# Kernel optimization log

Hardware: AMD Instinct MI355X
Metric: run time of the kernel (lower is better)

## Reference

```python
import jax, jax.numpy as jnp
import numpy as np

# Dims: L layers, batch B, seq S, model dim D, heads H, ffn FF
L, B, S, D, H = 8, 2, 1024, 1024, 16
FF = 4 * D
HD = D // H
EPS = 1e-5  # torch LayerNorm default


def setup_inputs() -> dict:
    key = jax.random.key(0)
    ks = jax.random.split(key, 6)
    g = lambda k, shape, s: jax.random.normal(k, shape, jnp.float32) * s
    return {
        "x": g(ks[0], (B, S, D), 1.0),
        # True = masked out (code passes ~attn_mask to F.sdpa): causal mask
        "attn_mask": jnp.triu(jnp.ones((S, S), bool), 1),
        "qkv_w": g(ks[1], (L, 3 * D, D), 0.02),
        "qkv_b": jnp.zeros((L, 3 * D), jnp.float32),
        "out_w": g(ks[2], (L, D, D), 0.02),
        "out_b": jnp.zeros((L, D), jnp.float32),
        "w1": g(ks[3], (L, FF, D), 0.02),
        "b1": jnp.zeros((L, FF), jnp.float32),
        "w2": g(ks[4], (L, D, FF), 0.02),
        "b2": jnp.zeros((L, D), jnp.float32),
        "ln1_w": jnp.ones((L, D), jnp.float32),
        "ln1_b": jnp.zeros((L, D), jnp.float32),
        "ln2_w": jnp.ones((L, D), jnp.float32),
        "ln2_b": jnp.zeros((L, D), jnp.float32),
    }


def _layer_norm(x, w, b):
    m = jnp.mean(x, axis=-1, keepdims=True)
    v = jnp.var(x, axis=-1, keepdims=True)
    return (x - m) * jax.lax.rsqrt(v + EPS) * w + b


def _block(x, mask, qw, qb, ow, ob, w1, b1, w2, b2, l1w, l1b, l2w, l2b):
    # fused QKV projection: [B,S,3D]
    qkv = jnp.einsum("bsd,ed->bse", x, qw) + qb
    q, k, v = jnp.split(qkv, 3, axis=-1)
    k_cache, v_cache = k, v  # caches are stored pre-head-split [B,S,D]
    to_heads = lambda t: t.reshape(B, S, H, HD).transpose(0, 2, 1, 3)
    qh, kh, vh = to_heads(q), to_heads(k), to_heads(v)
    scores = jnp.einsum("bhqd,bhkd->bhqk", qh, kh) / jnp.sqrt(jnp.float32(HD))
    scores = jnp.where(mask, -jnp.inf, scores)  # mask True = disallowed
    attn = jnp.einsum("bhqk,bhkd->bhqd", jax.nn.softmax(scores, axis=-1), vh)
    attn = attn.transpose(0, 2, 1, 3).reshape(B, S, D)
    attn = jnp.einsum("bsd,ed->bse", attn, ow) + ob
    # post-LN residual + ReLU MLP + post-LN (padding_mask=None branch)
    x = _layer_norm(x + attn, l1w, l1b)
    h = jnp.einsum("bsf,df->bsd", jax.nn.relu(jnp.einsum("bsd,fd->bsf", x, w1) + b1), w2) + b2
    x = _layer_norm(x + h, l2w, l2b)
    return x, k_cache, v_cache


def reference(x, attn_mask, qkv_w, qkv_b, out_w, out_b, w1, b1, w2, b2,
              ln1_w, ln1_b, ln2_w, ln2_b):
    def step(carry, p):
        xc = carry
        xo, kc, vc = _block(xc, attn_mask, *p)
        return xo, (kc, vc)

    params = (qkv_w, qkv_b, out_w, out_b, w1, b1, w2, b2,
              ln1_w, ln1_b, ln2_w, ln2_b)
    x_out, (k_cache, v_cache) = jax.lax.scan(step, x, params)
    return x_out, k_cache, v_cache
```

## Files before the change

kernel.cpp:

```cpp
#include <hip/hip_runtime.h>
#include <cstdint>
#include <cstddef>
#include <math.h>

#define LL  8
#define BB  2
#define SS  1024
#define DD  1024
#define HH  16
#define HD  64
#define FFD 4096
#define BSD (BB*SS*DD)

typedef __attribute__((ext_vector_type(4))) float f32x4;
typedef __attribute__((ext_vector_type(8))) short bf16x8;
typedef __attribute__((ext_vector_type(4))) short bf16x4;

__device__ __forceinline__ unsigned short f2bf(float f) {
    unsigned u = __float_as_uint(f);
    unsigned r = (u + 0x7fffu + ((u >> 16) & 1u)) >> 16;
    return (unsigned short)r;
}
__device__ __forceinline__ float bf2f(unsigned short u) {
    return __uint_as_float((unsigned)u << 16);
}

#define GLD16(gsrc, ldst) \
    __builtin_amdgcn_global_load_lds((const __attribute__((address_space(1))) void*)(gsrc), \
                                     (__attribute__((address_space(3))) void*)(ldst), 16, 0, 0)

__global__ __launch_bounds__(256)
void cvt_bf16(const float* __restrict__ in, unsigned short* __restrict__ out)
{
    size_t i = (size_t)blockIdx.x * 256 + threadIdx.x;
    float4 v = *(const float4*)(in + i * 4);
    ushort4 o;
    o.x = f2bf(v.x); o.y = f2bf(v.y); o.z = f2bf(v.z); o.w = f2bf(v.w);
    *(ushort4*)(out + i * 4) = o;
}

__global__ __launch_bounds__(256)
void cvt_x(const float* __restrict__ in, float* __restrict__ outf,
           unsigned short* __restrict__ outb)
{
    size_t i = (size_t)blockIdx.x * 256 + threadIdx.x;
    float4 v = *(const float4*)(in + i * 4);
    *(float4*)(outf + i * 4) = v;
    ushort4 o;
    o.x = f2bf(v.x); o.y = f2bf(v.y); o.z = f2bf(v.z); o.w = f2bf(v.w);
    *(ushort4*)(outb + i * 4) = o;
}

__global__ __launch_bounds__(512)
void gemm_bf16(const unsigned short* __restrict__ A, const unsigned short* __restrict__ W,
               const float* __restrict__ bias,
               float* __restrict__ C, unsigned short* __restrict__ Cb,
               float* __restrict__ Ck, float* __restrict__ Cv,
               unsigned short* __restrict__ Kb16, unsigned short* __restrict__ Vb16,
               int M, int N, int klen, int mode)
{
    __shared__ unsigned short lds[2][2 * 128 * 64];

    const int tid  = threadIdx.x;
    const int m0   = blockIdx.y * 128;
    const int n0   = blockIdx.x * 128;
    const int kbase= blockIdx.z * klen;
    const int lane = tid & 63;
    const int w    = tid >> 6;
    const int wr   = w >> 2;
    const int wc   = w & 3;
    const int lr   = lane & 15;
    const int kq   = lane >> 4;

    const int K = (mode == 3) ? (klen * gridDim.z) : klen;
    const int T = klen >> 6;

    const int srow0 = tid >> 3;
    const int spc0  = tid & 7;
    const int slc0  = spc0 ^ (srow0 & 7);
    const int srow1 = (tid + 512) >> 3;
    const int spc1  = (tid + 512) & 7;
    const int slc1  = spc1 ^ (srow1 & 7);

    #define STAGE_TILE(ti, dst)                                                   \
        do {                                                                      \
            const int kc = kbase + (ti) * 64;                                     \
            GLD16(A + (size_t)(m0 + srow0) * K + kc + slc0 * 8, (dst) + tid * 8); \
            GLD16(A + (size_t)(m0 + srow1) * K + kc + slc1 * 8, (dst) + 4096 + tid * 8); \
            GLD16(W + (size_t)(n0 + srow0) * K + kc + slc0 * 8, (dst) + 8192 + tid * 8); \
            GLD16(W + (size_t)(n0 + srow1) * K + kc + slc1 * 8, (dst) + 12288 + tid * 8); \
        } while (0)

    f32x4 acc[4][2];
    #pragma unroll
    for (int i = 0; i < 4; ++i)
        #pragma unroll
        for (int j = 0; j < 2; ++j) {
            f32x4 z = {0.f, 0.f, 0.f, 0.f};
            acc[i][j] = z;
        }

    STAGE_TILE(0, lds[0]);
    STAGE_TILE(1, lds[1]);

    for (int t = 0; t < T; ++t) {
        unsigned short* cb = lds[t & 1];

        if (t == T - 1) {
            asm volatile("s_waitcnt vmcnt(0)\n\ts_barrier" ::: "memory");
        } else {
            asm volatile("s_waitcnt vmcnt(4)\n\ts_barrier" ::: "memory");
        }

        bf16x8 a[4], b[2];
        #pragma unroll
        for (int mf = 0; mf < 4; ++mf) {
            const int r = wr * 64 + mf * 16 + lr;
            const int pc = kq ^ (r & 7);
            a[mf] = *(const bf16x8*)(cb + r * 64 + pc * 8);
        }
        #pragma unroll
        for (int nf = 0; nf < 2; ++nf) {
            const int r = wc * 32 + nf * 16 + lr;
            const int pc = kq ^ (r & 7);
            b[nf] = *(const bf16x8*)(cb + 8192 + r * 64 + pc * 8);
        }
        bf16x8 a2[4], b2[2];
        #pragma unroll
        for (int mf = 0; mf < 4; ++mf) {
            const int r = wr * 64 + mf * 16 + lr;
            const int pc = (4 + kq) ^ (r & 7);
            a2[mf] = *(const bf16x8*)(cb + r * 64 + pc * 8);
        }
        #pragma unroll
        for (int nf = 0; nf < 2; ++nf) {
            const int r = wc * 32 + nf * 16 + lr;
            const int pc = (4 + kq) ^ (r & 7);
            b2[nf] = *(const bf16x8*)(cb + 8192 + r * 64 + pc * 8);
        }

        asm volatile("s_waitcnt lgkmcnt(0)\n\ts_barrier" ::: "memory");

        if (t + 2 < T) STAGE_TILE(t + 2, cb);
        __builtin_amdgcn_sched_barrier(0);

        __builtin_amdgcn_s_setprio(1);
        #pragma unroll
        for (int mf = 0; mf < 4; ++mf)
            #pragma unroll
            for (int nf = 0; nf < 2; ++nf)
                acc[mf][nf] = __builtin_amdgcn_mfma_f32_16x16x32_bf16(
                    a[mf], b[nf], acc[mf][nf], 0, 0, 0);
        #pragma unroll
        for (int mf = 0; mf < 4; ++mf)
            #pragma unroll
            for (int nf = 0; nf < 2; ++nf)
                acc[mf][nf] = __builtin_amdgcn_mfma_f32_16x16x32_bf16(
                    a2[mf], b2[nf], acc[mf][nf], 0, 0, 0);
        __builtin_amdgcn_s_setprio(0);
    }
    #undef STAGE_TILE

    const int seg = n0 >> 10;
    #pragma unroll
    for (int nf = 0; nf < 2; ++nf) {
        const int cl = wc * 32 + nf * 16 + lr;
        const float bv = (mode == 3) ? 0.f : bias[n0 + cl];
        #pragma unroll
        for (int mf = 0; mf < 4; ++mf) {
            #pragma unroll
            for (int r = 0; r < 4; ++r) {
                const int row = m0 + wr * 64 + mf * 16 + kq * 4 + r;
                const float val = acc[mf][nf][r] + bv;
                if (mode == 2) {
                    const int col = (n0 & 1023) + cl;
                    float* dstf = (seg == 1) ? Ck : ((seg == 2) ? Cv : nullptr);
                    unsigned short* dstb = (seg == 0) ? Cb : ((seg == 1) ? Kb16 : Vb16);
                    if (dstf) dstf[(size_t)row * DD + col] = val;
                    dstb[(size_t)row * DD + col] = f2bf(val);
                } else if (mode == 1) {
                    Cb[(size_t)row * N + n0 + cl] = f2bf(fmaxf(val, 0.f));
                } else {
                    Cb[(size_t)blockIdx.z * M * N + (size_t)row * N + n0 + cl] = f2bf(val);
                }
            }
        }
    }
}

__global__ __launch_bounds__(512)
void attn_mfma(const unsigned short* __restrict__ Qb, const unsigned short* __restrict__ Kb,
               const unsigned short* __restrict__ Vb, unsigned short* __restrict__ ctxb)
{
    const int qt = blockIdx.x;
    const int h  = blockIdx.y;
    const int b  = blockIdx.z;
    const int tid  = threadIdx.x;
    const int lane = tid & 63;
    const int w    = tid >> 6;
    const int lr   = lane & 15;
    const int hi   = lane >> 4;

    __shared__ unsigned short smem[(64 + 64 + 8 * 16) * 68];
    unsigned short* Ks = smem;
    unsigned short* Vt = smem + 64 * 68;
    unsigned short* Pl = smem + 128 * 68 + w * 16 * 68;

    const int qg0 = qt * 128 + w * 16;

    bf16x8 qa[2];
    {
        const unsigned short* qp = Qb + ((size_t)(b * SS + qg0 + lr)) * DD + h * HD;
        qa[0] = *(const bf16x8*)(qp + hi * 8);
        qa[1] = *(const bf16x8*)(qp + 32 + hi * 8);
    }

    f32x4 accO[4];
    #pragma unroll
    for (int t = 0; t < 4; ++t) { f32x4 z = {0.f,0.f,0.f,0.f}; accO[t] = z; }
    float m_run[4], l_run[4];
    #pragma unroll
    for (int r = 0; r < 4; ++r) { m_run[r] = -INFINITY; l_run[r] = 0.f; }

    const int nch = 2 * qt + 2;
    for (int c = 0; c < nch; ++c) {
        __syncthreads();
        const unsigned short* kb = Kb + ((size_t)(b * SS + c * 64)) * DD + h * HD;
        const unsigned short* vb = Vb + ((size_t)(b * SS + c * 64)) * DD + h * HD;
        {
            int r  = tid >> 3, ch = tid & 7;
            bf16x8 kv = *(const bf16x8*)(kb + (size_t)r * DD + ch * 8);
            *(bf16x4*)(Ks + r * 68 + ch * 8)     = __builtin_shufflevector(kv, kv, 0,1,2,3);
            *(bf16x4*)(Ks + r * 68 + ch * 8 + 4) = __builtin_shufflevector(kv, kv, 4,5,6,7);
            int k  = tid & 63, d0 = (tid >> 6) * 8;
            bf16x8 vv = *(const bf16x8*)(vb + (size_t)k * DD + d0);
            #pragma unroll
            for (int j = 0; j < 8; ++j)
                Vt[(d0 + j) * 68 + k] = (unsigned short)vv[j];
        }
        __syncthreads();

        f32x4 sa[4];
        #pragma unroll
        for (int t = 0; t < 4; ++t) { f32x4 z = {0.f,0.f,0.f,0.f}; sa[t] = z; }
        #pragma unroll
        for (int t = 0; t < 4; ++t) {
            #pragma unroll
            for (int s = 0; s < 2; ++s) {
                const unsigned short* bp = Ks + (t * 16 + lr) * 68 + s * 32 + hi * 8;
                bf16x4 b0 = *(const bf16x4*)bp;
                bf16x4 b1 = *(const bf16x4*)(bp + 4);
                bf16x8 bb = __builtin_shufflevector(b0, b1, 0,1,2,3,4,5,6,7);
                sa[t] = __builtin_amdgcn_mfma_f32_16x16x32_bf16(qa[s], bb, sa[t], 0, 0, 0);
            }
        }
        #pragma unroll
        for (int t = 0; t < 4; ++t) {
            #pragma unroll
            for (int r = 0; r < 4; ++r) {
                const int kg = c * 64 + t * 16 + lr;
                const int qg = qg0 + hi * 4 + r;
                sa[t][r] = (kg > qg) ? -1e30f : sa[t][r] * 0.125f;
            }
        }
        #pragma unroll
        for (int r = 0; r < 4; ++r) {
            float mx = fmaxf(fmaxf(sa[0][r], sa[1][r]), fmaxf(sa[2][r], sa[3][r]));
            mx = fmaxf(mx, __shfl_xor(mx, 1));
            mx = fmaxf(mx, __shfl_xor(mx, 2));
            mx = fmaxf(mx, __shfl_xor(mx, 4));
            mx = fmaxf(mx, __shfl_xor(mx, 8));
            const float mn = fmaxf(m_run[r], mx);
            float sum = 0.f;
            #pragma unroll
            for (int t = 0; t < 4; ++t) {
                float p = __expf(sa[t][r] - mn);
                sa[t][r] = p;
                sum += p;
            }
            sum += __shfl_xor(sum, 1);
            sum += __shfl_xor(sum, 2);
            sum += __shfl_xor(sum, 4);
            sum += __shfl_xor(sum, 8);
            const float sc = __expf(m_run[r] - mn);
            l_run[r] = l_run[r] * sc + sum;
            m_run[r] = mn;
            #pragma unroll
            for (int t = 0; t < 4; ++t) accO[t][r] *= sc;
        }
        #pragma unroll
        for (int t = 0; t < 4; ++t)
            #pragma unroll
            for (int r = 0; r < 4; ++r)
                Pl[(hi * 4 + r) * 68 + t * 16 + lr] = f2bf(sa[t][r]);

        #pragma unroll
        for (int s = 0; s < 2; ++s) {
            const unsigned short* ap = Pl + lr * 68 + s * 32 + hi * 8;
            bf16x4 a0 = *(const bf16x4*)ap;
            bf16x4 a1 = *(const bf16x4*)(ap + 4);
            bf16x8 aa = __builtin_shufflevector(a0, a1, 0,1,2,3,4,5,6,7);
            #pragma unroll
            for (int t = 0; t < 4; ++t) {
                const unsigned short* bp = Vt + (t * 16 + lr) * 68 + s * 32 + hi * 8;
                bf16x4 b0 = *(const bf16x4*)bp;
                bf16x4 b1 = *(const bf16x4*)(bp + 4);
                bf16x8 bb = __builtin_shufflevector(b0, b1, 0,1,2,3,4,5,6,7);
                accO[t] = __builtin_amdgcn_mfma_f32_16x16x32_bf16(aa, bb, accO[t], 0, 0, 0);
            }
        }
    }

    float inv[4];
    #pragma unroll
    for (int r = 0; r < 4; ++r) inv[r] = 1.f / l_run[r];

    __syncthreads();
    float* Of = (float*)smem;
    #pragma unroll
    for (int t = 0; t < 4; ++t)
        #pragma unroll
        for (int r = 0; r < 4; ++r)
            Of[(w * 16 + hi * 4 + r) * 68 + t * 16 + lr] = accO[t][r] * inv[r];
    __syncthreads();
    #pragma unroll
    for (int i = 0; i < 2; ++i) {
        int e = tid + i * 512;
        int r = e >> 3, ch = e & 7;
        const float* src = Of + r * 68 + ch * 8;
        float4 v0 = *(const float4*)(src);
        float4 v1 = *(const float4*)(src + 4);
        bf16x8 o;
        o[0] = (short)f2bf(v0.x); o[1] = (short)f2bf(v0.y);
        o[2] = (short)f2bf(v0.z); o[3] = (short)f2bf(v0.w);
        o[4] = (short)f2bf(v1.x); o[5] = (short)f2bf(v1.y);
        o[6] = (short)f2bf(v1.z); o[7] = (short)f2bf(v1.w);
        *(bf16x8*)(ctxb + ((size_t)(b * SS + qt * 128 + r)) * DD + h * HD + ch * 8) = o;
    }
}

__global__ __launch_bounds__(256)
void ln_kernel(float* __restrict__ x, const unsigned short* __restrict__ P,
               const float* __restrict__ bias,
               const float* __restrict__ w, const float* __restrict__ b,
               unsigned short* __restrict__ xb)
{
    const size_t PS = (size_t)BSD;
    const int row = blockIdx.x;
    const int t   = threadIdx.x;
    const int d0  = t * 4;
    float* xr = x + (size_t)row * DD;
    unsigned short* xbr = xb + (size_t)row * DD;
    const size_t base = (size_t)row * DD + d0;

    float4 xv = *(const float4*)(xr + d0);
    float4 bv = *(const float4*)(bias + d0);
    float z[4] = {xv.x + bv.x, xv.y + bv.y, xv.z + bv.z, xv.w + bv.w};
    #pragma unroll
    for (int p = 0; p < 4; ++p) {
        ushort4 pv = *(const ushort4*)(P + base + p * PS);
        z[0] += bf2f(pv.x); z[1] += bf2f(pv.y); z[2] += bf2f(pv.z); z[3] += bf2f(pv.w);
    }
    float s = z[0] + z[1] + z[2] + z[3];
    float ss = z[0]*z[0] + z[1]*z[1] + z[2]*z[2] + z[3]*z[3];

    #pragma unroll
    for (int off = 32; off; off >>= 1) {
        s  += __shfl_down(s, off);
        ss += __shfl_down(ss, off);
    }
    __shared__ float sbuf[4], ssbuf[4];
    const int wave = t >> 6, lane = t & 63;
    if (lane == 0) { sbuf[wave] = s; ssbuf[wave] = ss; }
    __syncthreads();
    if (t == 0) {
        float S = 0.f, SSum = 0.f;
        #pragma unroll
        for (int i = 0; i < 4; ++i) { S += sbuf[i]; SSum += ssbuf[i]; }
        float mean = S * (1.f / 1024.f);
        float var  = SSum * (1.f / 1024.f) - mean * mean;
        sbuf[0]  = mean;
        ssbuf[0] = rsqrtf(var + 1e-5f);
    }
    __syncthreads();
    const float mean = sbuf[0], rstd = ssbuf[0];

    float4 wv = *(const float4*)(w + d0);
    float4 bb = *(const float4*)(b + d0);
    float o0 = (z[0] - mean) * rstd * wv.x + bb.x;
    float o1 = (z[1] - mean) * rstd * wv.y + bb.y;
    float o2 = (z[2] - mean) * rstd * wv.z + bb.z;
    float o3 = (z[3] - mean) * rstd * wv.w + bb.w;
    *(float4*)(xr + d0) = make_float4(o0, o1, o2, o3);
    ushort4 ob4;
    ob4.x = f2bf(o0); ob4.y = f2bf(o1); ob4.z = f2bf(o2); ob4.w = f2bf(o3);
    *(ushort4*)(xbr + d0) = ob4;
}

extern "C" void kernel_launch(void* const* d_in, const int* in_sizes, int n_in,
                              void* d_out, int out_size, void* d_ws, size_t ws_size,
                              hipStream_t stream)
{
    const float* x_in  = (const float*)d_in[0];
    const float* qkv_w = (const float*)d_in[2];
    const float* qkv_b = (const float*)d_in[3];
    const float* out_w = (const float*)d_in[4];
    const float* out_b = (const float*)d_in[5];
    const float* w1    = (const float*)d_in[6];
    const float* b1    = (const float*)d_in[7];
    const float* w2    = (const float*)d_in[8];
    const float* b2    = (const float*)d_in[9];
    const float* ln1w  = (const float*)d_in[10];
    const float* ln1b  = (const float*)d_in[11];
    const float* ln2w  = (const float*)d_in[12];
    const float* ln2b  = (const float*)d_in[13];

    float* out_x = (float*)d_out;
    float* out_k = out_x + (size_t)BSD;
    float* out_v = out_k + (size_t)LL * BSD;

    const size_t MEG = 1024 * 1024;
    float* ws = (float*)d_ws;
    float*          xbuf  = ws;
    unsigned short* part16= (unsigned short*)(ws + 2 * MEG);
    unsigned short* xb16  = (unsigned short*)(ws + 6 * MEG);
    unsigned short* ctxb  = (unsigned short*)(ws + 7 * MEG);
    unsigned short* hb16  = (unsigned short*)(ws + 8 * MEG);
    unsigned short* qb16  = hb16;
    unsigned short* kb16  = hb16 + 2 * MEG;
    unsigned short* vb16  = hb16 + 4 * MEG;
    unsigned short* wAll  = (unsigned short*)(ws + 12 * MEG);

    unsigned short* qkvW = wAll;
    unsigned short* outW = wAll + 24 * MEG;
    unsigned short* w1W  = wAll + 32 * MEG;
    unsigned short* w2W  = wAll + 64 * MEG;

    cvt_bf16<<<24 * MEG / 1024, 256, 0, stream>>>(qkv_w, qkvW);
    cvt_bf16<<< 8 * MEG / 1024, 256, 0, stream>>>(out_w, outW);
    cvt_bf16<<<32 * MEG / 1024, 256, 0, stream>>>(w1,    w1W);
    cvt_bf16<<<32 * MEG / 1024, 256, 0, stream>>>(w2,    w2W);
    cvt_x<<<BSD / 1024, 256, 0, stream>>>(x_in, xbuf, xb16);

    const int M = BB * SS;

    for (int l = 0; l < LL; ++l) {
        const float* qb  = qkv_b + (size_t)l * 3 * DD;
        const float* ob  = out_b + (size_t)l * DD;
        const float* b1l = b1    + (size_t)l * FFD;
        const float* b2l = b2    + (size_t)l * DD;
        const unsigned short* qwl = qkvW + (size_t)l * 3 * DD * DD;
        const unsigned short* owl = outW + (size_t)l * DD * DD;
        const unsigned short* w1l = w1W  + (size_t)l * FFD * DD;
        const unsigned short* w2l = w2W  + (size_t)l * DD * FFD;
        float* kc = out_k + (size_t)l * BSD;
        float* vc = out_v + (size_t)l * BSD;

        gemm_bf16<<<dim3(3 * DD / 128, M / 128, 1), 512, 0, stream>>>(
            xb16, qwl, qb, nullptr, qb16, kc, vc, kb16, vb16, M, 3 * DD, DD, 2);

        attn_mfma<<<dim3(SS / 128, HH, BB), 512, 0, stream>>>(qb16, kb16, vb16, ctxb);

        gemm_bf16<<<dim3(DD / 128, M / 128, 4), 512, 0, stream>>>(
            ctxb, owl, nullptr, nullptr, part16, nullptr, nullptr, nullptr, nullptr,
            M, DD, DD / 4, 3);

        ln_kernel<<<M, 256, 0, stream>>>(xbuf, part16, ob,
                                         ln1w + (size_t)l * DD, ln1b + (size_t)l * DD, xb16);

        gemm_bf16<<<dim3(FFD / 128, M / 128, 1), 512, 0, stream>>>(
            xb16, w1l, b1l, nullptr, hb16, nullptr, nullptr, nullptr, nullptr,
            M, FFD, DD, 1);

        gemm_bf16<<<dim3(DD / 128, M / 128, 4), 512, 0, stream>>>(
            hb16, w2l, nullptr, nullptr, part16, nullptr, nullptr, nullptr, nullptr,
            M, DD, FFD / 4, 3);

        ln_kernel<<<M, 256, 0, stream>>>(xbuf, part16, b2l,
                                         ln2w + (size_t)l * DD, ln2b + (size_t)l * DD, xb16);
    }

    hipMemcpyAsync(out_x, xbuf, (size_t)BSD * sizeof(float),
                   hipMemcpyDeviceToDevice, stream);
}
```

Before: 1.284 ms.

## Widen attention key tile to 128 and add XCD-aware block swizzle

The attention kernel now processes 128 keys per iteration instead of 64, which halves the number of loop iterations, barriers and online-softmax rescales per query tile, at the cost of more LDS and registers. A block-index swizzle groups consecutive workgroups onto the same XCD for both the GEMM and attention kernels to improve L2 reuse of shared tiles. The larger score array (8 tiles) may raise register pressure and reduce occupancy. The swizzle assumes the workgroup count divides evenly by 8.

```diff
diff --git a/kernel.cpp b/kernel.cpp
--- a/kernel.cpp
+++ b/kernel.cpp
@@ -29,6 +29,17 @@
     __builtin_amdgcn_global_load_lds((const __attribute__((address_space(1))) void*)(gsrc), \
                                      (__attribute__((address_space(3))) void*)(ldst), 16, 0, 0)
 
+__device__ __forceinline__ void xcd_swizzle(int& bx, int& by)
+{
+    const int nx  = gridDim.x;
+    const int nwg = nx * gridDim.y;
+    const int flat = by * nx + bx;
+    const int cpx = nwg >> 3;
+    const int swz = (flat & 7) * cpx + (flat >> 3);
+    bx = swz % nx;
+    by = swz / nx;
+}
+
 __global__ __launch_bounds__(256)
 void cvt_bf16(const float* __restrict__ in, unsigned short* __restrict__ out)
 {
@@ -61,9 +72,12 @@
 {
     __shared__ unsigned short lds[2][2 * 128 * 64];
 
+    int bx = blockIdx.x, by = blockIdx.y;
+    xcd_swizzle(bx, by);
+
     const int tid  = threadIdx.x;
-    const int m0   = blockIdx.y * 128;
-    const int n0   = blockIdx.x * 128;
+    const int m0   = by * 128;
+    const int n0   = bx * 128;
     const int kbase= blockIdx.z * klen;
     const int lane = tid & 63;
     const int w    = tid >> 6;
@@ -192,8 +206,10 @@
 void attn_mfma(const unsigned short* __restrict__ Qb, const unsigned short* __restrict__ Kb,
                const unsigned short* __restrict__ Vb, unsigned short* __restrict__ ctxb)
 {
-    const int qt = blockIdx.x;
-    const int h  = blockIdx.y;
+    int bx = blockIdx.x, by = blockIdx.y;
+    xcd_swizzle(bx, by);
+    const int qt = bx;
+    const int h  = by;
     const int b  = blockIdx.z;
     const int tid  = threadIdx.x;
     const int lane = tid & 63;
@@ -201,10 +217,10 @@
     const int lr   = lane & 15;
     const int hi   = lane >> 4;
 
-    __shared__ unsigned short smem[(64 + 64 + 8 * 16) * 68];
+    __shared__ unsigned short smem[128 * 68 + 64 * 136 + 8 * 16 * 136];
     unsigned short* Ks = smem;
-    unsigned short* Vt = smem + 64 * 68;
-    unsigned short* Pl = smem + 128 * 68 + w * 16 * 68;
+    unsigned short* Vt = smem + 128 * 68;
+    unsigned short* Pl = smem + 128 * 68 + 64 * 136 + w * 16 * 136;
 
     const int qg0 = qt * 128 + w * 16;
 
@@ -222,29 +238,31 @@
     #pragma unroll
     for (int r = 0; r < 4; ++r) { m_run[r] = -INFINITY; l_run[r] = 0.f; }
 
-    const int nch = 2 * qt + 2;
+    const int nch = qt + 1;
     for (int c = 0; c < nch; ++c) {
         __syncthreads();
-        const unsigned short* kb = Kb + ((size_t)(b * SS + c * 64)) * DD + h * HD;
-        const unsigned short* vb = Vb + ((size_t)(b * SS + c * 64)) * DD + h * HD;
-        {
-            int r  = tid >> 3, ch = tid & 7;
+        const unsigned short* kb = Kb + ((size_t)(b * SS + c * 128)) * DD + h * HD;
+        const unsigned short* vb = Vb + ((size_t)(b * SS + c * 128)) * DD + h * HD;
+        #pragma unroll
+        for (int i = 0; i < 2; ++i) {
+            int e = tid + i * 512;
+            int r  = e >> 3, ch = e & 7;
             bf16x8 kv = *(const bf16x8*)(kb + (size_t)r * DD + ch * 8);
             *(bf16x4*)(Ks + r * 68 + ch * 8)     = __builtin_shufflevector(kv, kv, 0,1,2,3);
             *(bf16x4*)(Ks + r * 68 + ch * 8 + 4) = __builtin_shufflevector(kv, kv, 4,5,6,7);
-            int k  = tid & 63, d0 = (tid >> 6) * 8;
+            int k  = e & 127, d0 = (e >> 7) * 8;
             bf16x8 vv = *(const bf16x8*)(vb + (size_t)k * DD + d0);
             #pragma unroll
             for (int j = 0; j < 8; ++j)
-                Vt[(d0 + j) * 68 + k] = (unsigned short)vv[j];
+                Vt[(d0 + j) * 136 + k] = (unsigned short)vv[j];
         }
         __syncthreads();
 
-        f32x4 sa[4];
-        #pragma unroll
-        for (int t = 0; t < 4; ++t) { f32x4 z = {0.f,0.f,0.f,0.f}; sa[t] = z; }
-        #pragma unroll
-        for (int t = 0; t < 4; ++t) {
+        f32x4 sa[8];
+        #pragma unroll
+        for (int t = 0; t < 8; ++t) { f32x4 z = {0.f,0.f,0.f,0.f}; sa[t] = z; }
+        #pragma unroll
+        for (int t = 0; t < 8; ++t) {
             #pragma unroll
             for (int s = 0; s < 2; ++s) {
                 const unsigned short* bp = Ks + (t * 16 + lr) * 68 + s * 32 + hi * 8;
@@ -255,17 +273,19 @@
             }
         }
         #pragma unroll
-        for (int t = 0; t < 4; ++t) {
+        for (int t = 0; t < 8; ++t) {
             #pragma unroll
             for (int r = 0; r < 4; ++r) {
-                const int kg = c * 64 + t * 16 + lr;
+                const int kg = c * 128 + t * 16 + lr;
                 const int qg = qg0 + hi * 4 + r;
                 sa[t][r] = (kg > qg) ? -1e30f : sa[t][r] * 0.125f;
             }
         }
         #pragma unroll
         for (int r = 0; r < 4; ++r) {
-            float mx = fmaxf(fmaxf(sa[0][r], sa[1][r]), fmaxf(sa[2][r], sa[3][r]));
+            float mx = -INFINITY;
+            #pragma unroll
+            for (int t = 0; t < 8; ++t) mx = fmaxf(mx, sa[t][r]);
             mx = fmaxf(mx, __shfl_xor(mx, 1));
             mx = fmaxf(mx, __shfl_xor(mx, 2));
             mx = fmaxf(mx, __shfl_xor(mx, 4));
@@ -273,7 +293,7 @@
             const float mn = fmaxf(m_run[r], mx);
             float sum = 0.f;
             #pragma unroll
-            for (int t = 0; t < 4; ++t) {
+            for (int t = 0; t < 8; ++t) {
                 float p = __expf(sa[t][r] - mn);
                 sa[t][r] = p;
                 sum += p;
@@ -289,20 +309,20 @@
             for (int t = 0; t < 4; ++t) accO[t][r] *= sc;
         }
         #pragma unroll
-        for (int t = 0; t < 4; ++t)
+        for (int t = 0; t < 8; ++t)
             #pragma unroll
             for (int r = 0; r < 4; ++r)
-                Pl[(hi * 4 + r) * 68 + t * 16 + lr] = f2bf(sa[t][r]);
-
-        #pragma unroll
-        for (int s = 0; s < 2; ++s) {
-            const unsigned short* ap = Pl + lr * 68 + s * 32 + hi * 8;
+                Pl[(hi * 4 + r) * 136 + t * 16 + lr] = f2bf(sa[t][r]);
+
+        #pragma unroll
+        for (int s = 0; s < 4; ++s) {
+            const unsigned short* ap = Pl + lr * 136 + s * 32 + hi * 8;
             bf16x4 a0 = *(const bf16x4*)ap;
             bf16x4 a1 = *(const bf16x4*)(ap + 4);
             bf16x8 aa = __builtin_shufflevector(a0, a1, 0,1,2,3,4,5,6,7);
             #pragma unroll
             for (int t = 0; t < 4; ++t) {
-                const unsigned short* bp = Vt + (t * 16 + lr) * 68 + s * 32 + hi * 8;
+                const unsigned short* bp = Vt + (t * 16 + lr) * 136 + s * 32 + hi * 8;
                 bf16x4 b0 = *(const bf16x4*)bp;
                 bf16x4 b1 = *(const bf16x4*)(bp + 4);
                 bf16x8 bb = __builtin_shufflevector(b0, b1, 0,1,2,3,4,5,6,7);
```

Measured after the change: 1.246 ms. 1.03x faster.
